# Kernel tuning notes

Measured on AMD Instinct MI355X. Metric: run time of the kernel, lower is better.

Reference implementation:

```python
import jax, jax.numpy as jnp
import numpy as np

N_NODES = 100000
N_EDGES = 1600000
IN_DIM = 128


def _gcn_layer(x, W, b, src, dst, n):
    # PyG GCNConv (default): out_i = b + sum_{j in N(i) U {i}} d_j^{-1/2} d_i^{-1/2} (x_j W)
    # src/dst already include self-loops; deg computed over target index.
    h = x @ W                                                   # [N, F_out]
    deg = jax.ops.segment_sum(jnp.ones_like(dst, dtype=h.dtype), dst, num_segments=n)
    dinv = jnp.where(deg > 0, jax.lax.rsqrt(deg), 0.0)          # [N]
    norm = dinv[src] * dinv[dst]                                # [E+N]
    out = jax.ops.segment_sum(h[src] * norm[:, None], dst, num_segments=n)
    return out + b


def setup_inputs() -> dict:
    key = jax.random.key(0)
    ks = jax.random.split(key, 8)
    def glorot(k, shp):
        scale = np.sqrt(2.0 / (shp[0] + shp[1])).astype(np.float32)
        return jax.random.normal(k, shp, dtype=jnp.float32) * scale
    x = jax.random.normal(ks[0], (N_NODES, IN_DIM), dtype=jnp.float32)
    edge_index = jax.random.randint(ks[1], (2, N_EDGES), 0, N_NODES, dtype=jnp.int64)
    return {
        "x": x,
        "W1": glorot(ks[2], (IN_DIM, 16)), "b1": jnp.zeros((16,), jnp.float32),
        "W2": glorot(ks[3], (16, 32)),     "b2": jnp.zeros((32,), jnp.float32),
        "W3": glorot(ks[4], (32, 64)),     "b3": jnp.zeros((64,), jnp.float32),
        "Wl": glorot(ks[5], (64, 1)),      "bl": jnp.zeros((1,), jnp.float32),
        "edge_index": edge_index,
    }


def reference(x, W1, b1, W2, b2, W3, b3, Wl, bl, edge_index):
    n = x.shape[0]
    loops = jnp.arange(n, dtype=edge_index.dtype)
    src = jnp.concatenate([edge_index[0], loops])  # add self-loops (PyG default)
    dst = jnp.concatenate([edge_index[1], loops])
    h = jnp.tanh(_gcn_layer(x, W1, b1, src, dst, n))
    h = jnp.tanh(_gcn_layer(h, W2, b2, src, dst, n))
    h = jnp.tanh(_gcn_layer(h, W3, b3, src, dst, n))
    pooled = jnp.max(h, axis=0, keepdims=True)     # global_max_pool, batch=all-zeros -> [1, 64]
    return pooled @ Wl + bl                        # [1, 1]
```

## Files before the change

kernel.cpp:

```cpp
#include <hip/hip_runtime.h>
#include <cmath>


#define TPB 256
#define SCAN_EPB 1024

__device__ __forceinline__ unsigned f2ord(float x) {
    unsigned u = __float_as_uint(x);
    return (u & 0x80000000u) ? ~u : (u | 0x80000000u);
}
__device__ __forceinline__ float ord2f(unsigned o) {
    unsigned u = (o & 0x80000000u) ? (o & 0x7FFFFFFFu) : ~o;
    return __uint_as_float(u);
}
__device__ __forceinline__ unsigned short f2bf(float x) {
    unsigned u = __float_as_uint(x);
    return (unsigned short)((u + 0x7FFFu + ((u >> 16) & 1u)) >> 16);
}
__device__ __forceinline__ float bf2f(unsigned short b) {
    return __uint_as_float(((unsigned)b) << 16);
}

__global__ void k_detect(const int* __restrict__ ei, int* __restrict__ flag) {
    int nz = 0;
    for (int i = threadIdx.x; i < 1024; i += 64)
        nz |= (ei[2 * i + 1] != 0);
    int any = __any(nz);
    if (threadIdx.x == 0) *flag = any ? 0 : 1;
}

__global__ void k_convert(const int* __restrict__ ei, const int* __restrict__ flag,
                          int E, unsigned* __restrict__ pk, int* __restrict__ ed,
                          unsigned* __restrict__ deg8) {
    int e = blockIdx.x * TPB + threadIdx.x;
    if (e >= E) return;
    int s, d;
    if (*flag) {
        s = ei[2 * e];
        d = ei[2 * E + 2 * e];
    } else {
        s = ei[e];
        d = ei[E + e];
    }
    ed[e] = d;
    unsigned sh = 8u * (unsigned)(d & 3);
    unsigned old = atomicAdd(&deg8[d >> 2], 1u << sh);
    unsigned rank = (old >> sh) & 0xFFu;
    pk[e] = (rank << 24) | (unsigned)s;
}

__global__ void k_scan1(const unsigned* __restrict__ deg8, int n, int* __restrict__ rs,
                        int* __restrict__ bsum, float* __restrict__ dinv) {
    __shared__ int ts[TPB];
    int base = blockIdx.x * SCAN_EPB + threadIdx.x * 4;
    unsigned w = (base < n) ? deg8[base >> 2] : 0u;
    int d0 = w & 0xFF, d1 = (w >> 8) & 0xFF, d2 = (w >> 16) & 0xFF, d3 = (w >> 24) & 0xFF;
    if (base + 0 < n) dinv[base + 0] = rsqrtf((float)d0 + 1.0f);
    if (base + 1 < n) dinv[base + 1] = rsqrtf((float)d1 + 1.0f);
    if (base + 2 < n) dinv[base + 2] = rsqrtf((float)d2 + 1.0f);
    if (base + 3 < n) dinv[base + 3] = rsqrtf((float)d3 + 1.0f);
    int v0 = (base + 0 < n) ? (d0 + 7) & ~7 : 0;
    int v1 = (base + 1 < n) ? (d1 + 7) & ~7 : 0;
    int v2 = (base + 2 < n) ? (d2 + 7) & ~7 : 0;
    int v3 = (base + 3 < n) ? (d3 + 7) & ~7 : 0;
    int tsum = v0 + v1 + v2 + v3;
    ts[threadIdx.x] = tsum;
    __syncthreads();
    for (int off = 1; off < TPB; off <<= 1) {
        int t = (threadIdx.x >= off) ? ts[threadIdx.x - off] : 0;
        __syncthreads();
        ts[threadIdx.x] += t;
        __syncthreads();
    }
    int run = ts[threadIdx.x] - tsum;
    if (base + 0 < n) rs[base + 0] = run; run += v0;
    if (base + 1 < n) rs[base + 1] = run; run += v1;
    if (base + 2 < n) rs[base + 2] = run; run += v2;
    if (base + 3 < n) rs[base + 3] = run;
    if (threadIdx.x == TPB - 1) bsum[blockIdx.x] = ts[TPB - 1];
}

__global__ void k_scan2(int* __restrict__ bsum, int nblk) {
    __shared__ int ts[TPB];
    int v = (threadIdx.x < nblk) ? bsum[threadIdx.x] : 0;
    ts[threadIdx.x] = v;
    __syncthreads();
    for (int off = 1; off < TPB; off <<= 1) {
        int t = (threadIdx.x >= off) ? ts[threadIdx.x - off] : 0;
        __syncthreads();
        ts[threadIdx.x] += t;
        __syncthreads();
    }
    if (threadIdx.x == nblk - 1) bsum[255] = ts[threadIdx.x];
    __syncthreads();
    if (threadIdx.x < nblk) bsum[threadIdx.x] = ts[threadIdx.x] - v;
}

__global__ void k_scan3(int* __restrict__ rs, const int* __restrict__ bsum, int n) {
    int i = blockIdx.x * TPB + threadIdx.x;
    if (i < n) rs[i] += bsum[i >> 10];
    if (i == 0) rs[n] = bsum[255];
}

__global__ void k_fill(int* __restrict__ csr, int cap, int n) {
    int i = blockIdx.x * TPB + threadIdx.x;
    if (i < cap) csr[i] = n;
}

#define SC_BLK 2048
__global__ void k_scatter(const unsigned* __restrict__ pk, const int* __restrict__ ed,
                          const int* __restrict__ rs, int* __restrict__ csr,
                          int E, int chunk) {
    const int part = blockIdx.x & 7;
    const int lo = part * chunk, hi = lo + chunk;
    const int q = blockIdx.x >> 3;
    const int stride = (SC_BLK >> 3) * TPB;
    for (int e = q * TPB + threadIdx.x; e < E; e += stride) {
        int d = ed[e];
        if (d >= lo && d < hi) {
            unsigned w = pk[e];
            csr[rs[d] + (int)(w >> 24)] = (int)(w & 0xFFFFFFu);
        }
    }
}

__global__ void k_gemm1(const float* __restrict__ in, const float* __restrict__ W,
                        const float* __restrict__ dinv, unsigned short* __restrict__ h,
                        int n) {
    __shared__ float wsh[128 * 16];
    for (int i = threadIdx.x; i < 128 * 16; i += TPB) wsh[i] = W[i];
    __syncthreads();
    int node = blockIdx.x * TPB + threadIdx.x;
    if (node > n) return;
    float acc[16];
#pragma unroll
    for (int f = 0; f < 16; ++f) acc[f] = 0.0f;
    if (node < n) {
        const float4* xr = reinterpret_cast<const float4*>(in + (size_t)node * 128);
        for (int k0 = 0; k0 < 32; ++k0) {
            float4 xv = xr[k0];
#pragma unroll
            for (int j = 0; j < 4; ++j) {
                float xs = (&xv.x)[j];
                const float* wr = &wsh[(k0 * 4 + j) * 16];
#pragma unroll
                for (int f = 0; f < 16; ++f) acc[f] += xs * wr[f];
            }
        }
        float di = dinv[node];
#pragma unroll
        for (int f = 0; f < 16; ++f) acc[f] *= di;
    }
    unsigned ob[8];
#pragma unroll
    for (int i = 0; i < 8; ++i)
        ob[i] = (unsigned)f2bf(acc[2 * i]) | ((unsigned)f2bf(acc[2 * i + 1]) << 16);
    uint4* hp = reinterpret_cast<uint4*>(h + (size_t)node * 16);
    hp[0] = make_uint4(ob[0], ob[1], ob[2], ob[3]);
    hp[1] = make_uint4(ob[4], ob[5], ob[6], ob[7]);
}

template <int FIN, int FOUT>
__global__ void k_gemm(const float* __restrict__ in, const float* __restrict__ W,
                       const float* __restrict__ dinv, unsigned short* __restrict__ h,
                       int n) {
    __shared__ float xs[64 * (FIN + 1)];
    __shared__ float wsh[FIN * FOUT];
    const int node0 = blockIdx.x * 64;
    for (int i = threadIdx.x; i < FIN * FOUT; i += TPB) wsh[i] = W[i];
    for (int i = threadIdx.x; i < 64 * FIN; i += TPB) {
        int r = i / FIN, c = i % FIN;
        int node = node0 + r;
        xs[r * (FIN + 1) + c] = (node < n) ? in[node * FIN + c] : 0.0f;
    }
    __syncthreads();
    for (int i = threadIdx.x; i < 64 * FOUT; i += TPB) {
        int r = i / FOUT, f = i % FOUT;
        int node = node0 + r;
        float val = 0.0f;
        if (node < n) {
            float s = 0.0f;
#pragma unroll
            for (int k = 0; k < FIN; ++k)
                s += xs[r * (FIN + 1) + k] * wsh[k * FOUT + f];
            val = dinv[node] * s;
        }
        h[node * FOUT + f] = f2bf(val);
    }
}

template <int FOUT>
__global__ void k_gat(const int* __restrict__ rs, const int* __restrict__ csr,
                      const unsigned short* __restrict__ h, const float* __restrict__ dinv,
                      const float* __restrict__ b, float* __restrict__ out, int n) {
    constexpr int NPB = TPB / FOUT;
    int node = blockIdx.x * NPB + (int)(threadIdx.x / FOUT);
    int f = threadIdx.x & (FOUT - 1);
    if (node >= n) return;
    int beg = rs[node], end = rs[node + 1];
    float s = bf2f(h[node * FOUT + f]);
    for (int k = beg; k < end; k += 8) {
        int4 a = *reinterpret_cast<const int4*>(csr + k);
        int4 c = *reinterpret_cast<const int4*>(csr + k + 4);
        float s0 = bf2f(h[a.x * FOUT + f]);
        float s1 = bf2f(h[a.y * FOUT + f]);
        float s2 = bf2f(h[a.z * FOUT + f]);
        float s3 = bf2f(h[a.w * FOUT + f]);
        float s4 = bf2f(h[c.x * FOUT + f]);
        float s5 = bf2f(h[c.y * FOUT + f]);
        float s6 = bf2f(h[c.z * FOUT + f]);
        float s7 = bf2f(h[c.w * FOUT + f]);
        s += ((s0 + s1) + (s2 + s3)) + ((s4 + s5) + (s6 + s7));
    }
    float di = dinv[node];
    out[node * FOUT + f] = tanhf(b[f] + di * s);
}

__global__ void k_pool(const float* __restrict__ c, unsigned* __restrict__ pooled, int n) {
    int f = threadIdx.x & 63;
    int sub = threadIdx.x >> 6;
    int nb = gridDim.x;
    int rpb = (n + nb - 1) / nb;
    int start = blockIdx.x * rpb;
    int end = min(start + rpb, n);
    float m = -INFINITY;
    for (int node = start + sub; node < end; node += 4)
        m = fmaxf(m, c[node * 64 + f]);
    __shared__ float red[TPB];
    red[threadIdx.x] = m;
    __syncthreads();
    if (threadIdx.x < 64) {
        m = fmaxf(fmaxf(red[threadIdx.x], red[threadIdx.x + 64]),
                  fmaxf(red[threadIdx.x + 128], red[threadIdx.x + 192]));
        atomicMax(&pooled[threadIdx.x], f2ord(m));
    }
}

__global__ void k_final(const unsigned* __restrict__ pooled, const float* __restrict__ Wl,
                        const float* __restrict__ bl, float* __restrict__ out) {
    int f = threadIdx.x;
    float v = ord2f(pooled[f]) * Wl[f];
#pragma unroll
    for (int off = 32; off > 0; off >>= 1) v += __shfl_down(v, off);
    if (f == 0) out[0] = v + bl[0];
}

extern "C" void kernel_launch(void* const* d_in, const int* in_sizes, int n_in,
                              void* d_out, int out_size, void* d_ws, size_t ws_size,
                              hipStream_t stream) {
    const float* x  = (const float*)d_in[0];
    const float* W1 = (const float*)d_in[1];
    const float* b1 = (const float*)d_in[2];
    const float* W2 = (const float*)d_in[3];
    const float* b2 = (const float*)d_in[4];
    const float* W3 = (const float*)d_in[5];
    const float* b3 = (const float*)d_in[6];
    const float* Wl = (const float*)d_in[7];
    const float* bl = (const float*)d_in[8];
    const int*   ei = (const int*)d_in[9];

    const int n = in_sizes[0] / 128;
    const int E = in_sizes[9] / 2;
    const int CAP = E + 8 * n;
    const int chunk = (n + 7) / 8;
    const int nw8 = (n + 3) / 4;

    size_t off = 0;
    auto alloc = [&](size_t words) {
        size_t p = off;
        off += (words + 3) & ~(size_t)3;
        return (float*)d_ws + p;
    };
    int*      flag   = (int*)alloc(16);
    unsigned* deg8   = (unsigned*)alloc(nw8 + 64);
    unsigned* pooled = deg8 + nw8;
    int*      rs     = (int*)alloc(n + 1);
    int*      bsum   = (int*)alloc(256);
    float*    dinv   = alloc(n);
    unsigned* pk     = (unsigned*)alloc(E);
    int*      ed     = (int*)alloc(E);
    int*      csr    = (int*)alloc(CAP);
    unsigned short* bufA = (unsigned short*)alloc(((size_t)(n + 128) * 64 + 1) / 2);
    float*    bufC   = alloc((size_t)n * 64);

    const int nblk_scan = (n + SCAN_EPB - 1) / SCAN_EPB;

    hipMemsetAsync(deg8, 0, (size_t)(nw8 + 64) * sizeof(unsigned), stream);

    k_detect<<<1, 64, 0, stream>>>(ei, flag);
    k_convert<<<(E + TPB - 1) / TPB, TPB, 0, stream>>>(ei, flag, E, pk, ed, deg8);
    k_scan1<<<nblk_scan, TPB, 0, stream>>>(deg8, n, rs, bsum, dinv);
    k_scan2<<<1, TPB, 0, stream>>>(bsum, nblk_scan);
    k_scan3<<<(n + TPB - 1) / TPB, TPB, 0, stream>>>(rs, bsum, n);
    k_fill<<<(CAP + TPB - 1) / TPB, TPB, 0, stream>>>(csr, CAP, n);
    k_scatter<<<SC_BLK, TPB, 0, stream>>>(pk, ed, rs, csr, E, chunk);

    k_gemm1<<<(n + 1 + TPB - 1) / TPB, TPB, 0, stream>>>(x, W1, dinv, bufA, n);
    k_gat<16><<<(n + 15) / 16, TPB, 0, stream>>>(rs, csr, bufA, dinv, b1, bufC, n);

    k_gemm<16, 32><<<(n + 127) / 64, TPB, 0, stream>>>(bufC, W2, dinv, bufA, n);
    k_gat<32><<<(n + 7) / 8, TPB, 0, stream>>>(rs, csr, bufA, dinv, b2, bufC, n);

    k_gemm<32, 64><<<(n + 127) / 64, TPB, 0, stream>>>(bufC, W3, dinv, bufA, n);
    k_gat<64><<<(n + 3) / 4, TPB, 0, stream>>>(rs, csr, bufA, dinv, b3, bufC, n);

    k_pool<<<256, TPB, 0, stream>>>(bufC, pooled, n);
    k_final<<<1, 64, 0, stream>>>(pooled, Wl, bl, (float*)d_out);
}
```

Before: 414.3 us.

## Replace global atomic degree counting with per-block shared-memory histograms and column scan

Degree counting and per-edge rank assignment move from global packed-byte atomics to block-local shared-memory histograms, split into two node halves so each fits in LDS. A column scan over the per-block slabs then produces global degrees and per-block offsets, and the scatter combines the slab offset with the local rank. This is meant to remove contention on global atomics. In exchange it adds two extra kernels, a second pass over the edges, about 50 MB of slab traffic and a per-edge slab lookup during scatter.

```diff
diff --git a/kernel.cpp b/kernel.cpp
--- a/kernel.cpp
+++ b/kernel.cpp
@@ -4,6 +4,9 @@
 
 #define TPB 256
 #define SCAN_EPB 1024
+#define TPB_H 512
+#define SHE 14
+#define NBS 128
 
 __device__ __forceinline__ unsigned f2ord(float x) {
     unsigned u = __float_as_uint(x);
@@ -29,24 +32,77 @@
     if (threadIdx.x == 0) *flag = any ? 0 : 1;
 }
 
-__global__ void k_convert(const int* __restrict__ ei, const int* __restrict__ flag,
-                          int E, unsigned* __restrict__ pk, int* __restrict__ ed,
-                          unsigned* __restrict__ deg8) {
-    int e = blockIdx.x * TPB + threadIdx.x;
-    if (e >= E) return;
-    int s, d;
-    if (*flag) {
-        s = ei[2 * e];
-        d = ei[2 * E + 2 * e];
-    } else {
-        s = ei[e];
-        d = ei[E + e];
-    }
-    ed[e] = d;
-    unsigned sh = 8u * (unsigned)(d & 3);
-    unsigned old = atomicAdd(&deg8[d >> 2], 1u << sh);
-    unsigned rank = (old >> sh) & 0xFFu;
-    pk[e] = (rank << 24) | (unsigned)s;
+__global__ void k_histcvt(const int* __restrict__ ei, const int* __restrict__ flag,
+                          int E, int HALF, int nw0,
+                          int* __restrict__ es, int* __restrict__ ed,
+                          unsigned char* __restrict__ rank8, unsigned* __restrict__ slab0) {
+    __shared__ unsigned lh[12504];
+    for (int i = threadIdx.x; i < nw0; i += TPB_H) lh[i] = 0u;
+    __syncthreads();
+    const int b = blockIdx.x;
+    const int e0 = b << SHE, e1 = min(e0 + (1 << SHE), E);
+    const int i64 = *flag;
+    for (int e = e0 + threadIdx.x; e < e1; e += TPB_H) {
+        int s, d;
+        if (i64) { s = ei[2 * e]; d = ei[2 * E + 2 * e]; }
+        else     { s = ei[e];     d = ei[E + e]; }
+        es[e] = s;
+        ed[e] = d;
+        if (d < HALF) {
+            unsigned sh = 8u * (unsigned)(d & 3);
+            unsigned old = atomicAdd(&lh[d >> 2], 1u << sh);
+            rank8[e] = (unsigned char)((old >> sh) & 0xFFu);
+        }
+    }
+    __syncthreads();
+    unsigned* sl = slab0 + (size_t)b * nw0;
+    for (int i = threadIdx.x; i < nw0; i += TPB_H) sl[i] = lh[i];
+}
+
+__global__ void k_hist1(const int* __restrict__ ed, int E, int HALF, int nw1,
+                        unsigned char* __restrict__ rank8, unsigned* __restrict__ slab1) {
+    __shared__ unsigned lh[12504];
+    for (int i = threadIdx.x; i < nw1; i += TPB_H) lh[i] = 0u;
+    __syncthreads();
+    const int b = blockIdx.x;
+    const int e0 = b << SHE, e1 = min(e0 + (1 << SHE), E);
+    for (int e = e0 + threadIdx.x; e < e1; e += TPB_H) {
+        int d = ed[e];
+        if (d >= HALF) {
+            int dl = d - HALF;
+            unsigned sh = 8u * (unsigned)(dl & 3);
+            unsigned old = atomicAdd(&lh[dl >> 2], 1u << sh);
+            rank8[e] = (unsigned char)((old >> sh) & 0xFFu);
+        }
+    }
+    __syncthreads();
+    unsigned* sl = slab1 + (size_t)b * nw1;
+    for (int i = threadIdx.x; i < nw1; i += TPB_H) sl[i] = lh[i];
+}
+
+__global__ void k_colscan(unsigned* __restrict__ slab0, unsigned* __restrict__ slab1,
+                          int nw0, int nw1, int nb, unsigned* __restrict__ deg8) {
+    int w = blockIdx.x * TPB + threadIdx.x;
+    if (w < nw0) {
+        unsigned sum = 0;
+        unsigned* p = slab0 + w;
+        for (int b = 0; b < nb; ++b) {
+            unsigned t = p[(size_t)b * nw0];
+            p[(size_t)b * nw0] = sum;
+            sum += t;
+        }
+        deg8[w] = sum;
+    } else if (w < nw0 + nw1) {
+        int wl = w - nw0;
+        unsigned sum = 0;
+        unsigned* p = slab1 + wl;
+        for (int b = 0; b < nb; ++b) {
+            unsigned t = p[(size_t)b * nw1];
+            p[(size_t)b * nw1] = sum;
+            sum += t;
+        }
+        deg8[nw0 + wl] = sum;
+    }
 }
 
 __global__ void k_scan1(const unsigned* __restrict__ deg8, int n, int* __restrict__ rs,
@@ -108,9 +164,13 @@
 }
 
 #define SC_BLK 2048
-__global__ void k_scatter(const unsigned* __restrict__ pk, const int* __restrict__ ed,
-                          const int* __restrict__ rs, int* __restrict__ csr,
-                          int E, int chunk) {
+__global__ void k_scatter(const int* __restrict__ es, const int* __restrict__ ed,
+                          const unsigned char* __restrict__ rank8,
+                          const int* __restrict__ rs,
+                          const unsigned* __restrict__ slab0,
+                          const unsigned* __restrict__ slab1,
+                          int* __restrict__ csr, int E, int chunk,
+                          int HALF, int nw0, int nw1) {
     const int part = blockIdx.x & 7;
     const int lo = part * chunk, hi = lo + chunk;
     const int q = blockIdx.x >> 3;
@@ -118,8 +178,13 @@
     for (int e = q * TPB + threadIdx.x; e < E; e += stride) {
         int d = ed[e];
         if (d >= lo && d < hi) {
-            unsigned w = pk[e];
-            csr[rs[d] + (int)(w >> 24)] = (int)(w & 0xFFFFFFu);
+            int b = e >> SHE;
+            unsigned w;
+            int dl;
+            if (d < HALF) { dl = d;        w = slab0[(size_t)b * nw0 + (dl >> 2)]; }
+            else          { dl = d - HALF; w = slab1[(size_t)b * nw1 + (dl >> 2)]; }
+            int base = (int)((w >> (8u * (unsigned)(dl & 3))) & 0xFFu);
+            csr[rs[d] + base + (int)rank8[e]] = es[e];
         }
     }
 }
@@ -264,6 +329,10 @@
     const int CAP = E + 8 * n;
     const int chunk = (n + 7) / 8;
     const int nw8 = (n + 3) / 4;
+    const int HALF = ((n / 2) + 3) & ~3;
+    const int nw0 = HALF >> 2;
+    const int nw1 = nw8 - nw0;
+    const int nbh = (E + (1 << SHE) - 1) >> SHE;
 
     size_t off = 0;
     auto alloc = [&](size_t words) {
@@ -277,23 +346,29 @@
     int*      rs     = (int*)alloc(n + 1);
     int*      bsum   = (int*)alloc(256);
     float*    dinv   = alloc(n);
-    unsigned* pk     = (unsigned*)alloc(E);
+    int*      es     = (int*)alloc(E);
     int*      ed     = (int*)alloc(E);
+    unsigned char* rank8 = (unsigned char*)alloc((E + 3) / 4);
+    unsigned* slab0  = (unsigned*)alloc((size_t)NBS * nw0);
+    unsigned* slab1  = (unsigned*)alloc((size_t)NBS * nw1);
     int*      csr    = (int*)alloc(CAP);
     unsigned short* bufA = (unsigned short*)alloc(((size_t)(n + 128) * 64 + 1) / 2);
     float*    bufC   = alloc((size_t)n * 64);
 
     const int nblk_scan = (n + SCAN_EPB - 1) / SCAN_EPB;
 
-    hipMemsetAsync(deg8, 0, (size_t)(nw8 + 64) * sizeof(unsigned), stream);
+    hipMemsetAsync(pooled, 0, 64 * sizeof(unsigned), stream);
 
     k_detect<<<1, 64, 0, stream>>>(ei, flag);
-    k_convert<<<(E + TPB - 1) / TPB, TPB, 0, stream>>>(ei, flag, E, pk, ed, deg8);
+    k_histcvt<<<nbh, TPB_H, 0, stream>>>(ei, flag, E, HALF, nw0, es, ed, rank8, slab0);
+    k_hist1<<<nbh, TPB_H, 0, stream>>>(ed, E, HALF, nw1, rank8, slab1);
+    k_colscan<<<(nw0 + nw1 + TPB - 1) / TPB, TPB, 0, stream>>>(slab0, slab1, nw0, nw1, nbh, deg8);
     k_scan1<<<nblk_scan, TPB, 0, stream>>>(deg8, n, rs, bsum, dinv);
     k_scan2<<<1, TPB, 0, stream>>>(bsum, nblk_scan);
     k_scan3<<<(n + TPB - 1) / TPB, TPB, 0, stream>>>(rs, bsum, n);
     k_fill<<<(CAP + TPB - 1) / TPB, TPB, 0, stream>>>(csr, CAP, n);
-    k_scatter<<<SC_BLK, TPB, 0, stream>>>(pk, ed, rs, csr, E, chunk);
+    k_scatter<<<SC_BLK, TPB, 0, stream>>>(es, ed, rank8, rs, slab0, slab1,
+                                          csr, E, chunk, HALF, nw0, nw1);
 
     k_gemm1<<<(n + 1 + TPB - 1) / TPB, TPB, 0, stream>>>(x, W1, dinv, bufA, n);
     k_gat<16><<<(n + 15) / 16, TPB, 0, stream>>>(rs, csr, bufA, dinv, b1, bufC, n);
```

New measurement: 405.7 us. 2.1% less time.
